# Kernel tuning notes

Measured on AMD Instinct MI355X. Metric: run time of the kernel, lower is better.

The kernel has to match this reference:

```python
import jax, jax.numpy as jnp
import numpy as np

B, C, T = 8, 256, 8192
CALC, H = 256, 4
D = CALC // H  # head dim = 64
EPS = 1e-5


def setup_inputs() -> dict:
    key = jax.random.key(0)
    ks = jax.random.split(key, 5)
    return {
        "x": jax.random.normal(ks[0], (B, C, T), dtype=jnp.float32),
        "W_prenet": jax.random.normal(ks[1], (3 * CALC, C), dtype=jnp.float32) * 0.05,
        "W_proj": jax.random.normal(ks[2], (C, CALC), dtype=jnp.float32) * 0.05,
        "b_proj": jax.random.normal(ks[3], (C,), dtype=jnp.float32) * 0.05,
        "scale": jax.random.normal(ks[4], (1,), dtype=jnp.float32),
        "gamma": jnp.ones((C,), dtype=jnp.float32),
        "beta": jnp.zeros((C,), dtype=jnp.float32),
    }


def reference(x, W_prenet, W_proj, b_proj, scale, gamma, beta):
    residual = x
    # 1x1 conv prenet: [B, 3*CALC, T]
    h = jnp.einsum('oc,bct->bot', W_prenet, x)
    # split heads: channels grouped as H blocks of 3*D, then chunk into q/k/v of D each
    h = h.reshape(B, H, 3 * D, T)
    q = h[:, :, :D, :]            # [B,H,D,T]
    k = h[:, :, D:2 * D, :]
    v = h[:, :, 2 * D:, :]
    # softmax over time on keys (with the module's +1e-5 shift)
    k = jax.nn.softmax(k + EPS, axis=3)
    # keys @ values^T : [B,H,Dk,Dv]
    kv = jnp.einsum('bhdt,bhet->bhde', k, v)
    # kv^T @ queries  : [B,H,Dv,T]
    ctx = jnp.einsum('bhde,bhdt->bhet', kv, q)
    ctx = ctx.reshape(B, CALC, T)
    # 1x1 conv projection + bias
    out = jnp.einsum('oc,bct->bot', W_proj, ctx) + b_proj[None, :, None]
    out = scale * out  # learnable scalar gate
    # dropout is identity in eval mode
    out = out + residual
    # LayerNorm over channel axis with per-channel affine
    mean = jnp.mean(out, axis=1, keepdims=True)
    var = jnp.var(out, axis=1, keepdims=True)
    out = (out - mean) * jax.lax.rsqrt(var + EPS)
    out = out * gamma[None, :, None] + beta[None, :, None]
    return out
```

## Files before the change

kernel.cpp:

```cpp
#include <hip/hip_runtime.h>
#include <hip/hip_bf16.h>
#include <math.h>

#define BB 8
#define CC 256
#define TT 8192
#define EPSF 1e-5f

typedef short v8s __attribute__((ext_vector_type(8)));
typedef float v4f __attribute__((ext_vector_type(4)));

#define MFMA(a, b, c) __builtin_amdgcn_mfma_f32_16x16x32_bf16((a), (b), (c), 0, 0, 0)


#define OFF_XT 0
#define OFF_WKV 8388608
#define OFF_WPJ 8454144
#define OFF_ZPART 8486912
#define OFF_KV 8617984
#define OFF_UPART 8749056
#define OFF_PT 8749056
#define OFF_MBF 9011200

__device__ __forceinline__ unsigned short f2bf(float f) {
  __hip_bfloat16 h = __float2bfloat16(f);
  return __builtin_bit_cast(unsigned short, h);
}
__device__ __forceinline__ float bf2f(unsigned short u) {
  return __bfloat162float(__builtin_bit_cast(__hip_bfloat16, u));
}

__device__ __forceinline__ void ldscpy16(unsigned short* lds_base,
                                         const unsigned short* g_lane) {
  __builtin_amdgcn_global_load_lds(
      (const __attribute__((address_space(1))) unsigned int*)(const void*)g_lane,
      (__attribute__((address_space(3))) unsigned int*)(void*)lds_base, 16, 0, 0);
}

__global__ __launch_bounds__(256) void kT_transpose(const float* __restrict__ x,
                                                    float* __restrict__ ws) {
  __shared__ float lsx[64 * 65];
  const int bi = blockIdx.x;
  const int b = bi >> 9;
  const int cseg = (bi >> 7) & 3;
  const int tseg = bi & 127;
  const int c0 = cseg * 64, t0 = tseg * 64;
  const int tid = threadIdx.x;
  {
    const int cl = tid >> 2, q4 = tid & 3;
    const float* xp = x + (size_t)b * CC * TT + (size_t)(c0 + cl) * TT + t0 + q4 * 16;
#pragma unroll
    for (int j = 0; j < 4; ++j) {
      const float4 v = reinterpret_cast<const float4*>(xp)[j];
      float* d = &lsx[cl * 65 + q4 * 16 + j * 4];
      d[0] = v.x; d[1] = v.y; d[2] = v.z; d[3] = v.w;
    }
  }
  __syncthreads();
  {
    const int tl = tid >> 2, cs = tid & 3;
    unsigned short ub[16];
#pragma unroll
    for (int j = 0; j < 16; ++j) ub[j] = f2bf(lsx[(cs * 16 + j) * 65 + tl]);
    unsigned short* xrow =
        (unsigned short*)(ws + OFF_XT) + ((size_t)b * TT + t0 + tl) * 256;
    const int m = tl & 7;
    const int j0 = cseg * 8 + cs * 2;
    *reinterpret_cast<int4*>(xrow + ((j0 + 0) ^ m) * 8) =
        *reinterpret_cast<int4*>(&ub[0]);
    *reinterpret_cast<int4*>(xrow + ((j0 + 1) ^ m) * 8) =
        *reinterpret_cast<int4*>(&ub[8]);
  }
}

__global__ void k0_pack(const float* __restrict__ Wpre,
                        const float* __restrict__ Wproj,
                        float* __restrict__ ws) {
  const int r = blockIdx.x;
  const int c = threadIdx.x;
  if (r < 512) {
    const int h = r >> 7, type = (r >> 6) & 1, d = r & 63;
    const int src = h * 192 + 64 + type * 64 + d;
    ((unsigned short*)(ws + OFF_WKV))[r * 256 + c] = f2bf(Wpre[(size_t)src * 256 + c]);
  } else {
    const int rr = r - 512;
    ((unsigned short*)(ws + OFF_WPJ))[rr * 256 + c] = f2bf(Wproj[(size_t)rr * 256 + c]);
  }
}

__global__ __launch_bounds__(512, 2) void k1_kv(float* __restrict__ ws) {
  __shared__ unsigned short lds[20480];

  const int tid = threadIdx.x;
  const int w = tid >> 6, lane = tid & 63, q = lane >> 4, cl = lane & 15;
  const int h = w >> 1, type = w & 1;
  const int bi = blockIdx.x;
  const int b = bi >> 6, chunk = bi & 63;
  const int t0 = chunk * 128;
  const unsigned short* xT =
      (const unsigned short*)(ws + OFF_XT) + (size_t)b * TT * 256;
  const unsigned short* wkv =
      (const unsigned short*)(ws + OFF_WKV) + (size_t)((h * 2 + type) * 64) * 256;
  unsigned short* ekb = &lds[h * 5120];
  unsigned short* vbb = &lds[h * 5120 + 2560];

  v4f Uacc[2][4];
#pragma unroll
  for (int i = 0; i < 2; ++i)
#pragma unroll
    for (int j = 0; j < 4; ++j) Uacc[i][j] = (v4f){0.f, 0.f, 0.f, 0.f};
  float zacc[4][4];
#pragma unroll
  for (int i = 0; i < 4; ++i)
#pragma unroll
    for (int j = 0; j < 4; ++j) zacc[i][j] = 0.f;

  for (int sub = 0; sub < 2; ++sub) {
    {
      const unsigned short* xsrc = xT + (size_t)(t0 + sub * 64) * 256 + lane * 8;
#pragma unroll
      for (int i = 0; i < 4; ++i) {
        const int p = w * 4 + i;
        ldscpy16(&lds[p * 512], xsrc + p * 512);
      }
    }
    __syncthreads();

    v4f acc[4][4];
#pragma unroll
    for (int i = 0; i < 4; ++i)
#pragma unroll
      for (int j = 0; j < 4; ++j) acc[i][j] = (v4f){0.f, 0.f, 0.f, 0.f};
#pragma unroll
    for (int ks = 0; ks < 8; ++ks) {
      v8s af[4], bfu[4];
#pragma unroll
      for (int rt = 0; rt < 4; ++rt)
        af[rt] = *(const v8s*)(wkv + (size_t)(rt * 16 + cl) * 256 + ks * 32 + q * 8);
#pragma unroll
      for (int ct = 0; ct < 4; ++ct) {
        const int t = ct * 16 + cl;
        bfu[ct] = *(const v8s*)&lds[t * 256 + (((ks * 4 + q) ^ (t & 7)) * 8)];
      }
#pragma unroll
      for (int rt = 0; rt < 4; ++rt)
#pragma unroll
        for (int ct = 0; ct < 4; ++ct)
          acc[rt][ct] = MFMA(af[rt], bfu[ct], acc[rt][ct]);
    }
    __syncthreads();

#pragma unroll
    for (int hp = 0; hp < 2; ++hp) {
      if (type == 0) {
#pragma unroll
        for (int rt = 0; rt < 4; ++rt)
#pragma unroll
          for (int cc = 0; cc < 2; ++cc) {
            const int ct = hp * 2 + cc;
#pragma unroll
            for (int reg = 0; reg < 4; ++reg) {
              const float e = __expf(acc[rt][ct][reg]);
              zacc[rt][reg] += e;
              ekb[(rt * 16 + q * 4 + reg) * 40 + cc * 16 + cl] = f2bf(e);
            }
          }
      } else {
#pragma unroll
        for (int rt = 0; rt < 4; ++rt)
#pragma unroll
          for (int cc = 0; cc < 2; ++cc) {
            const int ct = hp * 2 + cc;
#pragma unroll
            for (int reg = 0; reg < 4; ++reg)
              vbb[(rt * 16 + q * 4 + reg) * 40 + cc * 16 + cl] =
                  f2bf(acc[rt][ct][reg]);
          }
      }
      __syncthreads();
      {
        const int du0 = type * 32;
        v8s afu[2], bfu[4];
#pragma unroll
        for (int ur = 0; ur < 2; ++ur)
          afu[ur] = *(const v8s*)&ekb[(du0 + ur * 16 + cl) * 40 + q * 8];
#pragma unroll
        for (int uc = 0; uc < 4; ++uc)
          bfu[uc] = *(const v8s*)&vbb[(uc * 16 + cl) * 40 + q * 8];
#pragma unroll
        for (int ur = 0; ur < 2; ++ur)
#pragma unroll
          for (int uc = 0; uc < 4; ++uc)
            Uacc[ur][uc] = MFMA(afu[ur], bfu[uc], Uacc[ur][uc]);
      }
      __syncthreads();
    }
  }

  if (type == 0) {
#pragma unroll
    for (int m = 1; m < 16; m <<= 1)
#pragma unroll
      for (int rt = 0; rt < 4; ++rt)
#pragma unroll
        for (int reg = 0; reg < 4; ++reg)
          zacc[rt][reg] += __shfl_xor(zacc[rt][reg], m, 64);
    if (cl == 0) {
      for (int rt = 0; rt < 4; ++rt)
        for (int reg = 0; reg < 4; ++reg)
          ws[OFF_ZPART + (size_t)bi * 256 + h * 64 + rt * 16 + q * 4 + reg] =
              zacc[rt][reg];
    }
  }
  unsigned short* Up =
      (unsigned short*)(ws + OFF_UPART) + (size_t)bi * 16384 + h * 4096;
#pragma unroll
  for (int ur = 0; ur < 2; ++ur)
#pragma unroll
    for (int uc = 0; uc < 4; ++uc)
#pragma unroll
      for (int reg = 0; reg < 4; ++reg)
        Up[(type * 32 + ur * 16 + q * 4 + reg) * 64 + uc * 16 + cl] =
            f2bf(Uacc[ur][uc][reg]);
}

__global__ void k2_reduce_kv(float* __restrict__ ws) {
  const int bi = blockIdx.x;
  const int bh = bi >> 4, j = bi & 15;
  const int b = bh >> 2, h = bh & 3;
  const int tid = threadIdx.x;

  __shared__ float zinv[64];
  if (tid < 64) {
    float z = 0.f;
    for (int cb = 0; cb < 64; ++cb)
      z += ws[OFF_ZPART + (size_t)(b * 64 + cb) * 256 + h * 64 + tid];
    zinv[tid] = 1.0f / z;
  }
  __syncthreads();

  const int idx = j * 256 + tid;
  const int d = idx >> 6;
  const unsigned short* up = (const unsigned short*)(ws + OFF_UPART);
  float s = 0.f;
  for (int cb = 0; cb < 64; ++cb)
    s += bf2f(up[(size_t)(b * 64 + cb) * 16384 + h * 4096 + idx]);
  ws[OFF_KV + (size_t)(b * 4 + h) * 4096 + idx] = s * zinv[d];
}

__global__ void k3a_P(const float* __restrict__ Wpre, float* __restrict__ ws) {
  const int bi = blockIdx.x;
  const int b = bi >> 8, he = bi & 255;
  const int h = he >> 6, e = he & 63;
  const int c = threadIdx.x;
  const float* kvp = ws + OFF_KV + (size_t)(b * 4 + h) * 4096;
  float acc = 0.f;
#pragma unroll 8
  for (int d = 0; d < 64; ++d)
    acc += kvp[d * 64 + e] * Wpre[(size_t)(h * 192 + d) * 256 + c];
  ((unsigned short*)(ws + OFF_PT))[(size_t)b * 65536 + (size_t)c * 256 + he] =
      f2bf(acc);
}

__global__ __launch_bounds__(256, 2) void k3b_M(const float* __restrict__ scale,
                                                float* __restrict__ ws) {
  const int bi = blockIdx.x, b = bi >> 2, cg = bi & 3;
  const int tid = threadIdx.x, w = tid >> 6, lane = tid & 63, q = lane >> 4,
            cl = lane & 15;
  const unsigned short* wpj = (const unsigned short*)(ws + OFF_WPJ);
  const unsigned short* pt =
      (const unsigned short*)(ws + OFF_PT) + (size_t)b * 65536;
  v4f acc[4][4];
#pragma unroll
  for (int i = 0; i < 4; ++i)
#pragma unroll
    for (int j = 0; j < 4; ++j) acc[i][j] = (v4f){0.f, 0.f, 0.f, 0.f};
#pragma unroll
  for (int ks = 0; ks < 8; ++ks) {
    v8s af[4], bfu[4];
#pragma unroll
    for (int rt = 0; rt < 4; ++rt)
      af[rt] = *(const v8s*)(wpj + (size_t)(w * 64 + rt * 16 + cl) * 256 +
                             ks * 32 + q * 8);
#pragma unroll
    for (int ct = 0; ct < 4; ++ct)
      bfu[ct] = *(const v8s*)(pt + (size_t)(cg * 64 + ct * 16 + cl) * 256 +
                              ks * 32 + q * 8);
#pragma unroll
    for (int rt = 0; rt < 4; ++rt)
#pragma unroll
      for (int ct = 0; ct < 4; ++ct)
        acc[rt][ct] = MFMA(af[rt], bfu[ct], acc[rt][ct]);
  }
  const float s = scale[0];
  unsigned short* mbf = (unsigned short*)(ws + OFF_MBF);
#pragma unroll
  for (int rt = 0; rt < 4; ++rt)
#pragma unroll
    for (int ct = 0; ct < 4; ++ct)
#pragma unroll
      for (int reg = 0; reg < 4; ++reg) {
        const int o = w * 64 + rt * 16 + q * 4 + reg;
        const int c = cg * 64 + ct * 16 + cl;
        mbf[((size_t)b * 256 + o) * 256 + c] = f2bf(s * acc[rt][ct][reg]);
      }
}

__global__ __launch_bounds__(256, 2) void k4_proj_ln(
    const float* __restrict__ bproj, const float* __restrict__ scale,
    const float* __restrict__ gamma, const float* __restrict__ beta,
    const float* __restrict__ ws, float* __restrict__ out) {
  __shared__ unsigned short xs[16384];
  __shared__ float red1[256], red2[256], muA[64], rsA[64];
  const int bi = blockIdx.x, b = bi >> 7, tc = bi & 127;
  const int tg0 = tc * 64;
  const int tid = threadIdx.x, w = tid >> 6, lane = tid & 63, q = lane >> 4,
            cl = lane & 15;

  {
    const unsigned short* xsrc = (const unsigned short*)(ws + OFF_XT) +
                                 ((size_t)b * TT + tg0) * 256 + lane * 8;
#pragma unroll
    for (int i = 0; i < 8; ++i) {
      const int p = w * 8 + i;
      ldscpy16(&xs[p * 512], xsrc + p * 512);
    }
  }
  __syncthreads();

  const unsigned short* mbf =
      (const unsigned short*)(ws + OFF_MBF) + (size_t)b * 65536;
  v4f acc[4][4];
#pragma unroll
  for (int i = 0; i < 4; ++i)
#pragma unroll
    for (int j = 0; j < 4; ++j) acc[i][j] = (v4f){0.f, 0.f, 0.f, 0.f};
#pragma unroll
  for (int ks = 0; ks < 8; ++ks) {
    v8s af[4], bfu[4];
#pragma unroll
    for (int rt = 0; rt < 4; ++rt)
      af[rt] = *(const v8s*)(mbf + (size_t)(w * 64 + rt * 16 + cl) * 256 +
                             ks * 32 + q * 8);
#pragma unroll
    for (int ct = 0; ct < 4; ++ct) {
      const int t = ct * 16 + cl;
      bfu[ct] = *(const v8s*)&xs[t * 256 + (((ks * 4 + q) ^ (t & 7)) * 8)];
    }
#pragma unroll
    for (int rt = 0; rt < 4; ++rt)
#pragma unroll
      for (int ct = 0; ct < 4; ++ct)
        acc[rt][ct] = MFMA(af[rt], bfu[ct], acc[rt][ct]);
  }

  const float s = scale[0];
#pragma unroll
  for (int rt = 0; rt < 4; ++rt)
#pragma unroll
    for (int reg = 0; reg < 4; ++reg) {
      const int o = w * 64 + rt * 16 + q * 4 + reg;
      const float sb = s * bproj[o];
#pragma unroll
      for (int ct = 0; ct < 4; ++ct) {
        const int tl = ct * 16 + cl;
        acc[rt][ct][reg] +=
            sb + bf2f(xs[tl * 256 + (((o >> 3) ^ (tl & 7)) * 8) + (o & 7)]);
      }
    }

#pragma unroll
  for (int ct = 0; ct < 4; ++ct) {
    float s1 = 0.f, s2 = 0.f;
#pragma unroll
    for (int rt = 0; rt < 4; ++rt)
#pragma unroll
      for (int reg = 0; reg < 4; ++reg) {
        const float v = acc[rt][ct][reg];
        s1 += v;
        s2 += v * v;
      }
    s1 += __shfl_xor(s1, 16, 64);
    s1 += __shfl_xor(s1, 32, 64);
    s2 += __shfl_xor(s2, 16, 64);
    s2 += __shfl_xor(s2, 32, 64);
    if (q == 0) {
      red1[w * 64 + ct * 16 + cl] = s1;
      red2[w * 64 + ct * 16 + cl] = s2;
    }
  }
  __syncthreads();
  if (tid < 64) {
    const float s1 = red1[tid] + red1[64 + tid] + red1[128 + tid] + red1[192 + tid];
    const float s2 = red2[tid] + red2[64 + tid] + red2[128 + tid] + red2[192 + tid];
    const float mu = s1 * (1.f / 256.f);
    const float var = s2 * (1.f / 256.f) - mu * mu;
    muA[tid] = mu;
    rsA[tid] = rsqrtf(var + EPSF);
  }
  __syncthreads();

  float* ob = out + (size_t)b * (CC * TT) + tg0;
#pragma unroll
  for (int rt = 0; rt < 4; ++rt)
#pragma unroll
    for (int reg = 0; reg < 4; ++reg) {
      const int o = w * 64 + rt * 16 + q * 4 + reg;
      const float g = gamma[o], bt = beta[o];
#pragma unroll
      for (int ct = 0; ct < 4; ++ct) {
        const int tl = ct * 16 + cl;
        ob[(size_t)o * TT + tl] = (acc[rt][ct][reg] - muA[tl]) * rsA[tl] * g + bt;
      }
    }
}

extern "C" void kernel_launch(void* const* d_in, const int* in_sizes, int n_in,
                              void* d_out, int out_size, void* d_ws,
                              size_t ws_size, hipStream_t stream) {
  (void)in_sizes; (void)n_in; (void)out_size; (void)ws_size;
  const float* x = (const float*)d_in[0];
  const float* Wpre = (const float*)d_in[1];
  const float* Wproj = (const float*)d_in[2];
  const float* bproj = (const float*)d_in[3];
  const float* scale = (const float*)d_in[4];
  const float* gamma = (const float*)d_in[5];
  const float* beta = (const float*)d_in[6];
  float* out = (float*)d_out;
  float* ws = (float*)d_ws;

  hipLaunchKernelGGL(kT_transpose, dim3(4096), dim3(256), 0, stream, x, ws);
  hipLaunchKernelGGL(k0_pack, dim3(768), dim3(256), 0, stream, Wpre, Wproj, ws);
  hipLaunchKernelGGL(k1_kv, dim3(512), dim3(512), 0, stream, ws);
  hipLaunchKernelGGL(k2_reduce_kv, dim3(512), dim3(256), 0, stream, ws);
  hipLaunchKernelGGL(k3a_P, dim3(BB * 256), dim3(256), 0, stream, Wpre, ws);
  hipLaunchKernelGGL(k3b_M, dim3(32), dim3(256), 0, stream, scale, ws);
  hipLaunchKernelGGL(k4_proj_ln, dim3(BB * 128), dim3(256), 0, stream, bproj,
                     scale, gamma, beta, ws, out);
}
```

Baseline: 228.6 us.

## Fuse x transpose/bf16 conversion into kv and projection kernels

Drops the separate transpose kernel that wrote a bf16 time-major copy of x to workspace. Instead, k1_kv and k4_proj_ln each read fp32 x directly, convert it to bf16 and store it into swizzled LDS. This removes one full write and re-read of the transposed activation plus one launch, at the cost of reading fp32 x twice and doing the conversion inside the compute kernels. It also gives k1 a separate LDS buffer so one barrier can be dropped, and raises k4's launch-bounds occupancy hint from 2 to 4.

```diff
diff --git a/kernel.cpp b/kernel.cpp
--- a/kernel.cpp
+++ b/kernel.cpp
@@ -13,7 +13,6 @@
 #define MFMA(a, b, c) __builtin_amdgcn_mfma_f32_16x16x32_bf16((a), (b), (c), 0, 0, 0)
 
 
-#define OFF_XT 0
 #define OFF_WKV 8388608
 #define OFF_WPJ 8454144
 #define OFF_ZPART 8486912
@@ -28,49 +27,6 @@
 }
 __device__ __forceinline__ float bf2f(unsigned short u) {
   return __bfloat162float(__builtin_bit_cast(__hip_bfloat16, u));
-}
-
-__device__ __forceinline__ void ldscpy16(unsigned short* lds_base,
-                                         const unsigned short* g_lane) {
-  __builtin_amdgcn_global_load_lds(
-      (const __attribute__((address_space(1))) unsigned int*)(const void*)g_lane,
-      (__attribute__((address_space(3))) unsigned int*)(void*)lds_base, 16, 0, 0);
-}
-
-__global__ __launch_bounds__(256) void kT_transpose(const float* __restrict__ x,
-                                                    float* __restrict__ ws) {
-  __shared__ float lsx[64 * 65];
-  const int bi = blockIdx.x;
-  const int b = bi >> 9;
-  const int cseg = (bi >> 7) & 3;
-  const int tseg = bi & 127;
-  const int c0 = cseg * 64, t0 = tseg * 64;
-  const int tid = threadIdx.x;
-  {
-    const int cl = tid >> 2, q4 = tid & 3;
-    const float* xp = x + (size_t)b * CC * TT + (size_t)(c0 + cl) * TT + t0 + q4 * 16;
-#pragma unroll
-    for (int j = 0; j < 4; ++j) {
-      const float4 v = reinterpret_cast<const float4*>(xp)[j];
-      float* d = &lsx[cl * 65 + q4 * 16 + j * 4];
-      d[0] = v.x; d[1] = v.y; d[2] = v.z; d[3] = v.w;
-    }
-  }
-  __syncthreads();
-  {
-    const int tl = tid >> 2, cs = tid & 3;
-    unsigned short ub[16];
-#pragma unroll
-    for (int j = 0; j < 16; ++j) ub[j] = f2bf(lsx[(cs * 16 + j) * 65 + tl]);
-    unsigned short* xrow =
-        (unsigned short*)(ws + OFF_XT) + ((size_t)b * TT + t0 + tl) * 256;
-    const int m = tl & 7;
-    const int j0 = cseg * 8 + cs * 2;
-    *reinterpret_cast<int4*>(xrow + ((j0 + 0) ^ m) * 8) =
-        *reinterpret_cast<int4*>(&ub[0]);
-    *reinterpret_cast<int4*>(xrow + ((j0 + 1) ^ m) * 8) =
-        *reinterpret_cast<int4*>(&ub[8]);
-  }
 }
 
 __global__ void k0_pack(const float* __restrict__ Wpre,
@@ -88,8 +44,10 @@
   }
 }
 
-__global__ __launch_bounds__(512, 2) void k1_kv(float* __restrict__ ws) {
-  __shared__ unsigned short lds[20480];
+__global__ __launch_bounds__(512, 2) void k1_kv(const float* __restrict__ x,
+                                                float* __restrict__ ws) {
+  __shared__ unsigned short xs[16384];
+  __shared__ unsigned short ev[20480];
 
   const int tid = threadIdx.x;
   const int w = tid >> 6, lane = tid & 63, q = lane >> 4, cl = lane & 15;
@@ -97,12 +55,14 @@
   const int bi = blockIdx.x;
   const int b = bi >> 6, chunk = bi & 63;
   const int t0 = chunk * 128;
-  const unsigned short* xT =
-      (const unsigned short*)(ws + OFF_XT) + (size_t)b * TT * 256;
+  const float* xb = x + (size_t)b * (CC * TT);
   const unsigned short* wkv =
       (const unsigned short*)(ws + OFF_WKV) + (size_t)((h * 2 + type) * 64) * 256;
-  unsigned short* ekb = &lds[h * 5120];
-  unsigned short* vbb = &lds[h * 5120 + 2560];
+  unsigned short* ekb = &ev[h * 5120];
+  unsigned short* vbb = &ev[h * 5120 + 2560];
+
+  const int c8 = tid >> 4;
+  const int t4 = tid & 15;
 
   v4f Uacc[2][4];
 #pragma unroll
@@ -116,12 +76,22 @@
     for (int j = 0; j < 4; ++j) zacc[i][j] = 0.f;
 
   for (int sub = 0; sub < 2; ++sub) {
+    const int ts = t0 + sub * 64;
     {
-      const unsigned short* xsrc = xT + (size_t)(t0 + sub * 64) * 256 + lane * 8;
+      const float* xp = xb + (size_t)(c8 * 8) * TT + ts + t4 * 4;
+      float4 r[8];
+#pragma unroll
+      for (int j = 0; j < 8; ++j)
+        r[j] = *reinterpret_cast<const float4*>(xp + (size_t)j * TT);
 #pragma unroll
       for (int i = 0; i < 4; ++i) {
-        const int p = w * 4 + i;
-        ldscpy16(&lds[p * 512], xsrc + p * 512);
+        const int t = t4 * 4 + i;
+        unsigned short pk[8];
+#pragma unroll
+        for (int j = 0; j < 8; ++j)
+          pk[j] = f2bf(reinterpret_cast<const float*>(&r[j])[i]);
+        *reinterpret_cast<int4*>(&xs[t * 256 + ((c8 ^ (t & 7)) * 8)]) =
+            *reinterpret_cast<const int4*>(pk);
       }
     }
     __syncthreads();
@@ -140,7 +110,7 @@
 #pragma unroll
       for (int ct = 0; ct < 4; ++ct) {
         const int t = ct * 16 + cl;
-        bfu[ct] = *(const v8s*)&lds[t * 256 + (((ks * 4 + q) ^ (t & 7)) * 8)];
+        bfu[ct] = *(const v8s*)&xs[t * 256 + (((ks * 4 + q) ^ (t & 7)) * 8)];
       }
 #pragma unroll
       for (int rt = 0; rt < 4; ++rt)
@@ -148,7 +118,6 @@
         for (int ct = 0; ct < 4; ++ct)
           acc[rt][ct] = MFMA(af[rt], bfu[ct], acc[rt][ct]);
     }
-    __syncthreads();
 
 #pragma unroll
     for (int hp = 0; hp < 2; ++hp) {
@@ -193,7 +162,7 @@
           for (int uc = 0; uc < 4; ++uc)
             Uacc[ur][uc] = MFMA(afu[ur], bfu[uc], Uacc[ur][uc]);
       }
-      __syncthreads();
+      if (hp == 0) __syncthreads();
     }
   }
 
@@ -306,24 +275,39 @@
       }
 }
 
-__global__ __launch_bounds__(256, 2) void k4_proj_ln(
-    const float* __restrict__ bproj, const float* __restrict__ scale,
-    const float* __restrict__ gamma, const float* __restrict__ beta,
-    const float* __restrict__ ws, float* __restrict__ out) {
+__global__ __launch_bounds__(256, 4) void k4_proj_ln(
+    const float* __restrict__ x, const float* __restrict__ bproj,
+    const float* __restrict__ scale, const float* __restrict__ gamma,
+    const float* __restrict__ beta, const float* __restrict__ ws,
+    float* __restrict__ out) {
   __shared__ unsigned short xs[16384];
   __shared__ float red1[256], red2[256], muA[64], rsA[64];
   const int bi = blockIdx.x, b = bi >> 7, tc = bi & 127;
   const int tg0 = tc * 64;
   const int tid = threadIdx.x, w = tid >> 6, lane = tid & 63, q = lane >> 4,
             cl = lane & 15;
+  const float* xb = x + (size_t)b * (CC * TT);
 
   {
-    const unsigned short* xsrc = (const unsigned short*)(ws + OFF_XT) +
-                                 ((size_t)b * TT + tg0) * 256 + lane * 8;
-#pragma unroll
-    for (int i = 0; i < 8; ++i) {
-      const int p = w * 8 + i;
-      ldscpy16(&xs[p * 512], xsrc + p * 512);
+    const int c8 = tid >> 3;
+    const int t4 = tid & 7;
+#pragma unroll
+    for (int th = 0; th < 2; ++th) {
+      const float* xp = xb + (size_t)(c8 * 8) * TT + tg0 + th * 32 + t4 * 4;
+      float4 r[8];
+#pragma unroll
+      for (int j = 0; j < 8; ++j)
+        r[j] = *reinterpret_cast<const float4*>(xp + (size_t)j * TT);
+#pragma unroll
+      for (int i = 0; i < 4; ++i) {
+        const int t = th * 32 + t4 * 4 + i;
+        unsigned short pk[8];
+#pragma unroll
+        for (int j = 0; j < 8; ++j)
+          pk[j] = f2bf(reinterpret_cast<const float*>(&r[j])[i]);
+        *reinterpret_cast<int4*>(&xs[t * 256 + ((c8 ^ (t & 7)) * 8)]) =
+            *reinterpret_cast<const int4*>(pk);
+      }
     }
   }
   __syncthreads();
@@ -429,12 +413,11 @@
   float* out = (float*)d_out;
   float* ws = (float*)d_ws;
 
-  hipLaunchKernelGGL(kT_transpose, dim3(4096), dim3(256), 0, stream, x, ws);
   hipLaunchKernelGGL(k0_pack, dim3(768), dim3(256), 0, stream, Wpre, Wproj, ws);
-  hipLaunchKernelGGL(k1_kv, dim3(512), dim3(512), 0, stream, ws);
+  hipLaunchKernelGGL(k1_kv, dim3(512), dim3(512), 0, stream, x, ws);
   hipLaunchKernelGGL(k2_reduce_kv, dim3(512), dim3(256), 0, stream, ws);
   hipLaunchKernelGGL(k3a_P, dim3(BB * 256), dim3(256), 0, stream, Wpre, ws);
   hipLaunchKernelGGL(k3b_M, dim3(32), dim3(256), 0, stream, scale, ws);
-  hipLaunchKernelGGL(k4_proj_ln, dim3(BB * 128), dim3(256), 0, stream, bproj,
+  hipLaunchKernelGGL(k4_proj_ln, dim3(BB * 128), dim3(256), 0, stream, x, bproj,
                      scale, gamma, beta, ws, out);
 }
```

Result: slower. 239.7 us (+4.9%).
